# Kernel optimization log

Hardware: AMD Instinct MI355X
Metric: run time of the kernel (lower is better)

The kernel has to match this reference:

```python
import jax, jax.numpy as jnp
import numpy as np

BN_EPS = 1e-3  # Keras BatchNormalization default epsilon


def setup_inputs() -> dict:
    key = jax.random.key(0)
    ks = jax.random.split(key, 8)
    N, F, H, S, E = 30000, 16, 16, 8, 300000
    return {
        "x": jax.random.normal(ks[0], (N, F), dtype=jnp.float32),
        "e": jax.random.uniform(ks[1], (E, S), dtype=jnp.float32),
        "src": jax.random.randint(ks[2], (E,), 0, N),
        "dst": jax.random.randint(ks[3], (E,), 0, N),
        "Wk": jax.random.normal(ks[4], (S, F * H), dtype=jnp.float32) * 0.1,
        "bk": jnp.zeros((F * H,), dtype=jnp.float32),
        "Wr": jax.random.normal(ks[5], (F, H), dtype=jnp.float32) * 0.1,
        "br": jnp.zeros((H,), dtype=jnp.float32),
        "gamma": jnp.ones((H,), dtype=jnp.float32),
        "beta": jnp.zeros((H,), dtype=jnp.float32),
        "mmean": jnp.zeros((H,), dtype=jnp.float32),
        "mvar": jnp.ones((H,), dtype=jnp.float32),
        "Wd": jax.random.normal(ks[6], (H, 3), dtype=jnp.float32) * 0.1,
        "bd": jnp.zeros((3,), dtype=jnp.float32),
    }


def reference(x, e, src, dst, Wk, bk, Wr, br, gamma, beta, mmean, mvar, Wd, bd):
    N, F = x.shape
    H = Wr.shape[1]
    # ECCConv: per-edge filter generated from edge features -> [E, F, H]
    kernels = (e @ Wk + bk).reshape(e.shape[0], F, H)
    # message: gather source node feats, apply per-edge kernel
    msg = jnp.einsum('ef,efh->eh', x[src], kernels)  # [E, H]
    # scatter-sum aggregate to target nodes
    agg = jax.ops.segment_sum(msg, dst, num_segments=N)  # [N, H]
    h = jax.nn.relu(agg + x @ Wr + br)
    # BatchNormalization (inference: moving stats); Dropout = identity at eval
    h = (h - mmean) / jnp.sqrt(mvar + BN_EPS) * gamma + beta
    pooled = jnp.max(h, axis=0, keepdims=True)  # GlobalMaxPool, single mode -> [1, H]
    return pooled @ Wd + bd  # [1, 3]
```

## Files before the change

kernel.cpp:

```cpp
#include <hip/hip_runtime.h>

#define BN_EPS 1e-3f

__device__ __forceinline__ unsigned int f2k(float f) {
    unsigned int u = __float_as_uint(f);
    return (u & 0x80000000u) ? ~u : (u | 0x80000000u);
}
__device__ __forceinline__ float k2f(unsigned int u) {
    return __uint_as_float((u & 0x80000000u) ? (u & 0x7FFFFFFFu) : ~u);
}

template <int S, int F, int H>
__global__ void node_pre(const float* __restrict__ x,
                         const float* __restrict__ Wk,
                         const float* __restrict__ bk,
                         const float* __restrict__ Wr,
                         const float* __restrict__ br,
                         float* __restrict__ y,
                         float* __restrict__ yb,
                         float* __restrict__ base,
                         int N) {
    int t = blockIdx.x * blockDim.x + threadIdx.x;
    int n = t / H;
    int h = t % H;
    if (n >= N) return;

    float xf[F];
#pragma unroll
    for (int f = 0; f < F; ++f) xf[f] = x[n * F + f];

#pragma unroll
    for (int s = 0; s < S; ++s) {
        float acc = 0.f;
#pragma unroll
        for (int f = 0; f < F; ++f) acc += xf[f] * Wk[(s * F + f) * H + h];
        y[((size_t)n * S + s) * H + h] = acc;
    }

    float accb = 0.f, accr = 0.f;
#pragma unroll
    for (int f = 0; f < F; ++f) {
        accb += xf[f] * bk[f * H + h];
        accr += xf[f] * Wr[f * H + h];
    }
    yb[(size_t)n * H + h] = accb;
    base[(size_t)n * H + h] = accr + br[h];
}

template <int S, int H>
__global__ void edge_scatter(const float* __restrict__ efeat,
                             const int* __restrict__ src,
                             const int* __restrict__ dst,
                             const float* __restrict__ y,
                             const float* __restrict__ yb,
                             float* __restrict__ agg,
                             int E) {
    int t = blockIdx.x * blockDim.x + threadIdx.x;
    int edge = t / H;
    int h = t % H;
    if (edge >= E) return;

    int sn = src[edge];
    int dn = dst[edge];

    const float4* e4 = (const float4*)(efeat + (size_t)edge * S);
    float4 ea = e4[0];
    float4 eb = e4[1];
    float es[S] = {ea.x, ea.y, ea.z, ea.w, eb.x, eb.y, eb.z, eb.w};

    const float* yrow = y + (size_t)sn * S * H + h;
    float m = yb[(size_t)sn * H + h];
#pragma unroll
    for (int s = 0; s < S; ++s) m += es[s] * yrow[s * H];

    atomicAdd(&agg[(size_t)dn * H + h], m);
}

template <int H>
__global__ void bn_relu_max(const float* __restrict__ agg,
                            const float* __restrict__ base,
                            const float* __restrict__ gamma,
                            const float* __restrict__ beta,
                            const float* __restrict__ mmean,
                            const float* __restrict__ mvar,
                            unsigned int* __restrict__ pooled_u,
                            int N) {
    __shared__ unsigned int smax[H];
    if (threadIdx.x < H) smax[threadIdx.x] = 0u;
    __syncthreads();

    int t = blockIdx.x * blockDim.x + threadIdx.x;
    int stride = gridDim.x * blockDim.x;
    int h = t % H;

    float scale = gamma[h] * rsqrtf(mvar[h] + BN_EPS);
    float shift = beta[h] - mmean[h] * scale;

    float best = -INFINITY;
    int total = N * H;
    for (int i = t; i < total; i += stride) {
        float v = agg[i] + base[i];
        v = v > 0.f ? v : 0.f;
        v = v * scale + shift;
        best = fmaxf(best, v);
    }
    atomicMax(&smax[h], f2k(best));
    __syncthreads();
    if (threadIdx.x < H) atomicMax(&pooled_u[threadIdx.x], smax[threadIdx.x]);
}

template <int H>
__global__ void final_matvec(const unsigned int* __restrict__ pooled_u,
                             const float* __restrict__ Wd,
                             const float* __restrict__ bd,
                             float* __restrict__ out,
                             int HOUT) {
    int j = threadIdx.x;
    if (j >= HOUT) return;
    float acc = bd[j];
#pragma unroll
    for (int hh = 0; hh < H; ++hh) acc += k2f(pooled_u[hh]) * Wd[hh * HOUT + j];
    out[j] = acc;
}

extern "C" void kernel_launch(void* const* d_in, const int* in_sizes, int n_in,
                              void* d_out, int out_size, void* d_ws, size_t ws_size,
                              hipStream_t stream) {
    const float* x     = (const float*)d_in[0];
    const float* e     = (const float*)d_in[1];
    const int*   src   = (const int*)d_in[2];
    const int*   dst   = (const int*)d_in[3];
    const float* Wk    = (const float*)d_in[4];
    const float* bk    = (const float*)d_in[5];
    const float* Wr    = (const float*)d_in[6];
    const float* br    = (const float*)d_in[7];
    const float* gamma = (const float*)d_in[8];
    const float* beta  = (const float*)d_in[9];
    const float* mmean = (const float*)d_in[10];
    const float* mvar  = (const float*)d_in[11];
    const float* Wd    = (const float*)d_in[12];
    const float* bd    = (const float*)d_in[13];

    constexpr int S = 8, F = 16, H = 16;
    const int E = in_sizes[2];
    const int N = in_sizes[0] / F;
    const int HOUT = in_sizes[13];

    float* y    = (float*)d_ws;
    float* yb   = y    + (size_t)N * S * H;
    float* base = yb   + (size_t)N * H;
    float* agg  = base + (size_t)N * H;
    unsigned int* pooled_u = (unsigned int*)(agg + (size_t)N * H);

    hipMemsetAsync(agg, 0, (size_t)N * H * sizeof(float), stream);
    hipMemsetAsync(pooled_u, 0, H * sizeof(unsigned int), stream);

    const int T = 256;
    int nh = N * H;
    node_pre<S, F, H><<<(nh + T - 1) / T, T, 0, stream>>>(x, Wk, bk, Wr, br, y, yb, base, N);

    long long eh = (long long)E * H;
    edge_scatter<S, H><<<(int)((eh + T - 1) / T), T, 0, stream>>>(e, src, dst, y, yb, agg, E);

    bn_relu_max<H><<<1024, T, 0, stream>>>(agg, base, gamma, beta, mmean, mvar, pooled_u, N);

    final_matvec<H><<<1, 64, 0, stream>>>(pooled_u, Wd, bd, (float*)d_out, HOUT);
}
```

Measured before the change: 143.6 us.

## Fold bias row into y, seed agg with base, vectorize edge gather

The node-pre kernel now writes the bias projection as a ninth row of an interleaved y buffer and writes the root term straight into agg, so the memsets and the separate base buffer are removed. The pooled-max reset also moves into node_pre. Each edge now uses 4 threads, each loading float4 slices of y with nontemporal loads for the edge features, which cuts per-edge index and feature reloads. The cost is more registers per thread and four scalar atomics per thread instead of one.

Result: slower. 181.6 us (+26.5%).

```diff
diff --git a/kernel.cpp b/kernel.cpp
--- a/kernel.cpp
+++ b/kernel.cpp
@@ -1,6 +1,8 @@
 #include <hip/hip_runtime.h>
 
 #define BN_EPS 1e-3f
+
+typedef float vf4 __attribute__((ext_vector_type(4)));
 
 __device__ __forceinline__ unsigned int f2k(float f) {
     unsigned int u = __float_as_uint(f);
@@ -16,10 +18,12 @@
                          const float* __restrict__ bk,
                          const float* __restrict__ Wr,
                          const float* __restrict__ br,
-                         float* __restrict__ y,
-                         float* __restrict__ yb,
-                         float* __restrict__ base,
+                         float* __restrict__ y2,
+                         float* __restrict__ agg,
+                         unsigned int* __restrict__ pooled_u,
                          int N) {
+    if (blockIdx.x == 0 && threadIdx.x < H) pooled_u[threadIdx.x] = 0u;
+
     int t = blockIdx.x * blockDim.x + threadIdx.x;
     int n = t / H;
     int h = t % H;
@@ -29,12 +33,13 @@
 #pragma unroll
     for (int f = 0; f < F; ++f) xf[f] = x[n * F + f];
 
+    float* yrow = y2 + (size_t)n * (S + 1) * H + h;
 #pragma unroll
     for (int s = 0; s < S; ++s) {
         float acc = 0.f;
 #pragma unroll
         for (int f = 0; f < F; ++f) acc += xf[f] * Wk[(s * F + f) * H + h];
-        y[((size_t)n * S + s) * H + h] = acc;
+        yrow[s * H] = acc;
     }
 
     float accb = 0.f, accr = 0.f;
@@ -43,42 +48,50 @@
         accb += xf[f] * bk[f * H + h];
         accr += xf[f] * Wr[f * H + h];
     }
-    yb[(size_t)n * H + h] = accb;
-    base[(size_t)n * H + h] = accr + br[h];
+    yrow[S * H] = accb;
+    agg[(size_t)n * H + h] = accr + br[h];
 }
 
 template <int S, int H>
 __global__ void edge_scatter(const float* __restrict__ efeat,
                              const int* __restrict__ src,
                              const int* __restrict__ dst,
-                             const float* __restrict__ y,
-                             const float* __restrict__ yb,
+                             const float* __restrict__ y2,
                              float* __restrict__ agg,
                              int E) {
     int t = blockIdx.x * blockDim.x + threadIdx.x;
-    int edge = t / H;
-    int h = t % H;
+    int edge = t >> 2;
+    int h4 = t & 3;
     if (edge >= E) return;
 
     int sn = src[edge];
     int dn = dst[edge];
 
-    const float4* e4 = (const float4*)(efeat + (size_t)edge * S);
-    float4 ea = e4[0];
-    float4 eb = e4[1];
-    float es[S] = {ea.x, ea.y, ea.z, ea.w, eb.x, eb.y, eb.z, eb.w};
+    const vf4* e4 = (const vf4*)(efeat + (size_t)edge * S);
+    vf4 ea = __builtin_nontemporal_load(e4);
+    vf4 eb = __builtin_nontemporal_load(e4 + 1);
+    float es[S + 1] = {ea.x, ea.y, ea.z, ea.w, eb.x, eb.y, eb.z, eb.w, 1.0f};
 
-    const float* yrow = y + (size_t)sn * S * H + h;
-    float m = yb[(size_t)sn * H + h];
+    const vf4* yrow = (const vf4*)(y2 + (size_t)sn * (S + 1) * H) + h4;
+    vf4 m = {0.f, 0.f, 0.f, 0.f};
 #pragma unroll
-    for (int s = 0; s < S; ++s) m += es[s] * yrow[s * H];
+    for (int s = 0; s <= S; ++s) {
+        vf4 yv = yrow[s * (H / 4)];
+        m.x += es[s] * yv.x;
+        m.y += es[s] * yv.y;
+        m.z += es[s] * yv.z;
+        m.w += es[s] * yv.w;
+    }
 
-    atomicAdd(&agg[(size_t)dn * H + h], m);
+    float* ap = agg + (size_t)dn * H + h4 * 4;
+    atomicAdd(ap + 0, m.x);
+    atomicAdd(ap + 1, m.y);
+    atomicAdd(ap + 2, m.z);
+    atomicAdd(ap + 3, m.w);
 }
 
 template <int H>
 __global__ void bn_relu_max(const float* __restrict__ agg,
-                            const float* __restrict__ base,
                             const float* __restrict__ gamma,
                             const float* __restrict__ beta,
                             const float* __restrict__ mmean,
@@ -99,7 +112,7 @@
     float best = -INFINITY;
     int total = N * H;
     for (int i = t; i < total; i += stride) {
-        float v = agg[i] + base[i];
+        float v = agg[i];
         v = v > 0.f ? v : 0.f;
         v = v * scale + shift;
         best = fmaxf(best, v);
@@ -146,23 +159,20 @@
     const int N = in_sizes[0] / F;
     const int HOUT = in_sizes[13];
 
-    float* y    = (float*)d_ws;
-    float* yb   = y    + (size_t)N * S * H;
-    float* base = yb   + (size_t)N * H;
-    float* agg  = base + (size_t)N * H;
+    float* y2  = (float*)d_ws;
+    float* agg = y2 + (size_t)N * (S + 1) * H;
     unsigned int* pooled_u = (unsigned int*)(agg + (size_t)N * H);
-
-    hipMemsetAsync(agg, 0, (size_t)N * H * sizeof(float), stream);
-    hipMemsetAsync(pooled_u, 0, H * sizeof(unsigned int), stream);
 
     const int T = 256;
     int nh = N * H;
-    node_pre<S, F, H><<<(nh + T - 1) / T, T, 0, stream>>>(x, Wk, bk, Wr, br, y, yb, base, N);
+    node_pre<S, F, H><<<(nh + T - 1) / T, T, 0, stream>>>(
+        x, Wk, bk, Wr, br, y2, agg, pooled_u, N);
 
-    long long eh = (long long)E * H;
-    edge_scatter<S, H><<<(int)((eh + T - 1) / T), T, 0, stream>>>(e, src, dst, y, yb, agg, E);
+    long long et = (long long)E * 4;
+    edge_scatter<S, H><<<(int)((et + T - 1) / T), T, 0, stream>>>(
+        e, src, dst, y2, agg, E);
 
-    bn_relu_max<H><<<1024, T, 0, stream>>>(agg, base, gamma, beta, mmean, mvar, pooled_u, N);
+    bn_relu_max<H><<<1024, T, 0, stream>>>(agg, gamma, beta, mmean, mvar, pooled_u, N);
 
     final_matvec<H><<<1, 64, 0, stream>>>(pooled_u, Wd, bd, (float*)d_out, HOUT);
 }
```
